# Kernel tuning notes

Hardware: AMD Instinct MI355X
Metric: run time of the kernel (lower is better)

The kernel has to match this reference:

```python
import jax, jax.numpy as jnp
import numpy as np

EMBED = 768; HEADS = 12; MLP = 3072
WL_IN = 4        # activation bits (signed)
WL_W = 4         # weight bits (bit-sliced into 1-bit RRAM cells)
ADC = 5          # ADC precision for each analog partial sum
SUBARRAY = 128   # crossbar subArray rows
ONOFF = 10.0     # conductance on/off ratio
VARI = 0.02      # conductance variability
EPS = 1e-5


def _adc_quant(y, bits):
    # Linear ADC quantization over the full observed range.
    ymax = jnp.max(jnp.abs(y))
    step = ymax / (2 ** bits - 1)
    step = jnp.where(step > 0, step, jnp.ones_like(step))
    return jnp.round(y / step) * step


def _qlinear(x, W, b, key):
    # RRAM crossbar simulated linear layer. x: [T, Fin], W: [Fout, Fin].
    upper, lower = 1.0, 1.0 / ONOFF
    T, Fin = x.shape
    Fout = W.shape[0]
    Wlev = 2 ** WL_W - 1
    Xlev = 2 ** (WL_IN - 1) - 1
    # --- weight -> unsigned integer levels -> binary cell conductances ---
    wmax = jnp.max(jnp.abs(W))
    Wdec = jnp.round((W / wmax + 1.0) * 0.5 * Wlev).astype(jnp.int32)   # [Fout,Fin] in [0,Wlev]
    kb = jnp.arange(WL_W)
    wbits = ((Wdec[:, :, None] >> kb) & 1).astype(x.dtype)              # [Fout,Fin,K]
    noise = VARI * jax.random.normal(key, wbits.shape, dtype=x.dtype)   # conductance variability
    cond = (wbits * (upper - lower) + lower) * (1.0 + noise)
    dummy = 0.5 * (upper + lower)                                       # dummy column conductance
    # --- activation -> signed integer -> magnitude bit slices ---
    xmax = jnp.max(jnp.abs(x))
    Xq = jnp.round(x / xmax * Xlev).astype(jnp.int32)
    sgn = jnp.sign(Xq).astype(x.dtype)
    zb = jnp.arange(WL_IN - 1)
    xbits = ((jnp.abs(Xq)[:, :, None] >> zb) & 1).astype(x.dtype) * sgn[:, :, None]  # [T,Fin,Z]
    # --- subArray partitioning along input dim ---
    pad = (-Fin) % SUBARRAY
    if pad:
        xbits = jnp.pad(xbits, ((0, 0), (0, pad), (0, 0)))
        cond = jnp.pad(cond, ((0, 0), (0, pad), (0, 0)))
    nc = (Fin + pad) // SUBARRAY
    xb = xbits.reshape(T, nc, SUBARRAY, WL_IN - 1)
    cb = cond.reshape(Fout, nc, SUBARRAY, WL_W)
    # analog MAC per subarray, per (input bit z, weight cell k)
    partial = jnp.einsum('tcsz,ocsk->tcozk', xb, cb)                    # [T,nc,Fout,Z,K]
    dummyP = dummy * xb.sum(axis=2)                                     # [T,nc,Z]
    partialQ = _adc_quant(partial, ADC)
    dummyQ = _adc_quant(dummyP, ADC)
    net = partialQ - dummyQ[:, :, None, :, None]                        # recenter to signed weights
    scale = (2.0 ** zb)[:, None] * (2.0 ** kb)[None, :]                 # [Z,K] shift-add
    acc = jnp.einsum('tcozk,zk->to', net, scale)
    out = acc * (xmax / Xlev) * (2.0 * wmax / ((upper - lower) * Wlev))
    return out + b


def _layernorm(x, g, b):
    mu = jnp.mean(x, axis=-1, keepdims=True)
    var = jnp.var(x, axis=-1, keepdims=True)
    return (x - mu) * jax.lax.rsqrt(var + EPS) * g + b


def _attention(x, in_w, in_b, out_w, out_b):
    L, N, E = x.shape
    D = E // HEADS
    qkv = x @ in_w.T + in_b                                             # [L,N,3E]
    q, k, v = jnp.split(qkv, 3, axis=-1)
    q = q.reshape(L, N, HEADS, D)
    k = k.reshape(L, N, HEADS, D)
    v = v.reshape(L, N, HEADS, D)
    scores = jnp.einsum('lnhd,mnhd->nhlm', q, k) / jnp.sqrt(jnp.asarray(D, x.dtype))
    attn = jax.nn.softmax(scores, axis=-1)
    ctx = jnp.einsum('nhlm,mnhd->lnhd', attn, v).reshape(L, N, E)
    return ctx @ out_w.T + out_b


def setup_inputs() -> dict:
    key = jax.random.key(0)
    ks = jax.random.split(key, 8)
    s = 0.02
    return {
        'x': jax.random.normal(ks[0], (256, 2, EMBED), jnp.float32),
        'in_proj_w': s * jax.random.normal(ks[1], (3 * EMBED, EMBED), jnp.float32),
        'in_proj_b': jnp.zeros((3 * EMBED,), jnp.float32),
        'out_proj_w': s * jax.random.normal(ks[2], (EMBED, EMBED), jnp.float32),
        'out_proj_b': jnp.zeros((EMBED,), jnp.float32),
        'ln1_g': jnp.ones((EMBED,), jnp.float32),
        'ln1_b': jnp.zeros((EMBED,), jnp.float32),
        'W1': s * jax.random.normal(ks[3], (MLP, EMBED), jnp.float32),
        'b1': jnp.zeros((MLP,), jnp.float32),
        'W2': s * jax.random.normal(ks[4], (EMBED, MLP), jnp.float32),
        'b2': jnp.zeros((EMBED,), jnp.float32),
        'ln2_g': jnp.ones((EMBED,), jnp.float32),
        'ln2_b': jnp.zeros((EMBED,), jnp.float32),
    }


def reference(x, in_proj_w, in_proj_b, out_proj_w, out_proj_b,
              ln1_g, ln1_b, W1, b1, W2, b2, ln2_g, ln2_b):
    L, N, E = x.shape
    a = _attention(x, in_proj_w, in_proj_b, out_proj_w, out_proj_b)
    h = _layernorm(x + a, ln1_g, ln1_b)
    t = h.reshape(L * N, E)
    m = _qlinear(t, W1, b1, jax.random.key(1))
    m = jax.nn.gelu(m, approximate=False)   # torch nn.GELU default = exact erf
    m = _qlinear(m, W2, b2, jax.random.key(2))
    m = m.reshape(L, N, E)
    return _layernorm(h + m, ln2_g, ln2_b)
```

## Files before the change

kernel.cpp:

```cpp
#include <hip/hip_runtime.h>
#include <math.h>
#include <stdint.h>

#define TOK   512
#define EMB   768
#define QKVD  2304
#define NHEAD 12
#define HD    64
#define MLPD  3072
#define SUBA  128

#define OFF_QKV      0ull
#define OFF_SCORES   9437184ull
#define OFF_CTX      22020096ull
#define OFF_H1PRE    25165824ull
#define OFF_H1       26738688ull
#define OFF_M1       28311552ull
#define OFF_X2       34603008ull
#define OFF_M2       40894464ull
#define OFF_DQ1      42467328ull
#define OFF_DQ2      42504192ull
#define OFF_SCAL     42651648ull
#define OFF_NOISE1   42651712ull
#define OFF_NOISE2   80400448ull
#define OFF_SUMXB1   118149184ull
#define OFF_SUMXB2   118186048ull
#define OFF_WDEC1    118333504ull
#define OFF_WDEC2    120692800ull
#define OFF_XQT1     123052096ull
#define OFF_XQT2     123445312ull
#define WS_NEEDED    125018176ull


typedef float f32x2 __attribute__((ext_vector_type(2)));

__device__ __forceinline__ f32x2 pkfma(f32x2 a, f32x2 b, f32x2 c){
#if __has_builtin(__builtin_elementwise_fma)
  return __builtin_elementwise_fma(a, b, c);
#else
  f32x2 r; r.x = fmaf(a.x, b.x, c.x); r.y = fmaf(a.y, b.y, c.y); return r;
#endif
}

__device__ __forceinline__ void blockMaxAtomic(double v, unsigned long long* slot, double* red){
  int tid = threadIdx.x;
  red[tid] = v; __syncthreads();
  for (int st = 128; st > 0; st >>= 1){
    if (tid < st){ double o = red[tid+st]; if (o > red[tid]) red[tid] = o; }
    __syncthreads();
  }
  if (tid == 0) atomicMax(slot, (unsigned long long)__double_as_longlong(red[0]));
}

__device__ __forceinline__ double readSlot(const unsigned long long* s){
  return __longlong_as_double((long long)(*s));
}

__device__ __forceinline__ float xla_exp_f32(float _x){
  float x = fminf(_x, 88.3762626647950f);
  x = fmaxf(x, -88.3762626647949f);
  float m = floorf(fmaf(x, 1.44269504088896341f, 0.5f));
  float r = fmaf(m, -0.6931471805599453f, x);
  float r2 = __fmul_rn(r, r);
  float r3 = __fmul_rn(r2, r);
  float y  = fmaf(1.9875691500e-4f, r, 1.3981999507e-3f);
  float y1 = fmaf(4.1665795894e-2f, r, 1.6666665459e-1f);
  float y2 = __fadd_rn(r, 1.0f);
  y  = fmaf(y, r, 8.3334519073e-3f);
  y1 = fmaf(y1, r, 5.0000001201e-1f);
  y  = fmaf(y, r3, y1);
  y  = fmaf(y, r2, y2);
  int mi = (int)m;
  float two_m = __uint_as_float((unsigned)((mi + 127) << 23));
  float res = __fmul_rn(y, two_m);
  return fmaxf(res, _x);
}

__device__ __forceinline__ float xla_erf_f32(float v){
  float x = fmaxf(fminf(v, 4.0f), -4.0f);
  float x2 = __fmul_rn(x, x);
  float p = fmaf(x2, -2.72614225801306e-10f, 2.77068142495902e-08f);
  p = fmaf(x2, p, -2.10102402082508e-06f);
  p = fmaf(x2, p, -5.69250639462346e-05f);
  p = fmaf(x2, p, -7.34990630326855e-04f);
  p = fmaf(x2, p, -2.95459980854025e-03f);
  p = fmaf(x2, p, -1.60960333262415e-02f);
  p = __fmul_rn(x, p);
  float q = fmaf(x2, -1.45660718464996e-05f, -2.13374055278905e-04f);
  q = fmaf(x2, q, -1.68282697438203e-03f);
  q = fmaf(x2, q, -7.37332916720468e-03f);
  q = fmaf(x2, q, -1.42647390514189e-02f);
  return __fdiv_rn(p, q);
}

__device__ __forceinline__ uint32_t rotl32(uint32_t x, int r){ return (x << r) | (x >> (32 - r)); }

__device__ __forceinline__ void threefry2x32(uint32_t k0, uint32_t k1,
                                             uint32_t x0, uint32_t x1,
                                             uint32_t& o0, uint32_t& o1){
  uint32_t ks2 = k0 ^ k1 ^ 0x1BD11BDAu;
  x0 += k0; x1 += k1;
#define TF_R(r) { x0 += x1; x1 = rotl32(x1, r); x1 ^= x0; }
  TF_R(13) TF_R(15) TF_R(26) TF_R(6)
  x0 += k1; x1 += ks2 + 1u;
  TF_R(17) TF_R(29) TF_R(16) TF_R(24)
  x0 += ks2; x1 += k0 + 2u;
  TF_R(13) TF_R(15) TF_R(26) TF_R(6)
  x0 += k0; x1 += k1 + 3u;
  TF_R(17) TF_R(29) TF_R(16) TF_R(24)
  x0 += k1; x1 += ks2 + 4u;
  TF_R(13) TF_R(15) TF_R(26) TF_R(6)
  x0 += ks2; x1 += k0 + 5u;
#undef TF_R
  o0 = x0; o1 = x1;
}

__device__ float bits_to_noise(uint32_t bits){
  uint32_t fb = (bits >> 9) | 0x3f800000u;
  float f = __uint_as_float(fb);
  f = __fadd_rn(f, -1.0f);
  const float lo = -0.99999994f;
  float u = __fadd_rn(__fmul_rn(f, 2.0f), lo);
  u = fmaxf(lo, u);
  float x  = u;
  float xx = __fmul_rn(x, x);
  float nx = -xx;
  float l1p;
  if (fabsf(nx) < 1e-4f){
    l1p = __fmul_rn(__fadd_rn(__fmul_rn(-0.5f, nx), 1.0f), nx);
  } else {
    float u1 = __fadd_rn(nx, 1.0f);
    l1p = (float)log((double)u1);
  }
  float w = -l1p;
  float p;
  if (w < 5.0f){
    w = __fadd_rn(w, -2.5f);
    p = 2.81022636e-08f;
    p = __fadd_rn(3.43273939e-07f, __fmul_rn(p, w));
    p = __fadd_rn(-3.5233877e-06f,  __fmul_rn(p, w));
    p = __fadd_rn(-4.39150654e-06f, __fmul_rn(p, w));
    p = __fadd_rn(0.00021858087f,   __fmul_rn(p, w));
    p = __fadd_rn(-0.00125372503f,  __fmul_rn(p, w));
    p = __fadd_rn(-0.00417768164f,  __fmul_rn(p, w));
    p = __fadd_rn(0.246640727f,     __fmul_rn(p, w));
    p = __fadd_rn(1.50140941f,      __fmul_rn(p, w));
  } else {
    float sw = __fsqrt_rn(w);
    w = __fadd_rn(sw, -3.0f);
    p = -0.000200214257f;
    p = __fadd_rn(0.000100950558f, __fmul_rn(p, w));
    p = __fadd_rn(0.00134934322f,  __fmul_rn(p, w));
    p = __fadd_rn(-0.00367342844f, __fmul_rn(p, w));
    p = __fadd_rn(0.00573950773f,  __fmul_rn(p, w));
    p = __fadd_rn(-0.0076224613f,  __fmul_rn(p, w));
    p = __fadd_rn(0.00943887047f,  __fmul_rn(p, w));
    p = __fadd_rn(1.00167406f,     __fmul_rn(p, w));
    p = __fadd_rn(2.83297682f,     __fmul_rn(p, w));
  }
  float ei  = __fmul_rn(p, x);
  float nrm = __fmul_rn(1.41421354f, ei);
  return __fmul_rn(0.02f, nrm);
}

__global__ void absmax_f32_k(const float* p, int n, unsigned long long* slot){
  __shared__ double red[256];
  double m = 0.0;
  for (int i = blockIdx.x*256 + threadIdx.x; i < n; i += gridDim.x*256){
    double v = fabs((double)p[i]); if (v > m) m = v;
  }
  blockMaxAtomic(m, slot, red);
}

__global__ void noise_gen_k(uint32_t k0, uint32_t k1, unsigned int n, float* noise){
  unsigned int i = blockIdx.x*256u + threadIdx.x;
  if (i >= n) return;
  uint32_t o0, o1;
  threefry2x32(k0, k1, 0u, i, o0, o1);
  noise[i] = bits_to_noise(o0 ^ o1);
}

__global__ void wdec_gen_k(const float* W, int nW, const unsigned long long* wmax_slot,
                           unsigned char* Wdec){
  int i = blockIdx.x*256 + threadIdx.x;
  if (i >= nW) return;
  float wmax = (float)readSlot(wmax_slot);
  float d = __fdiv_rn(W[i], wmax);
  d = __fadd_rn(d, 1.0f);
  d = __fmul_rn(d, 0.5f);
  d = __fmul_rn(d, 15.0f);
  Wdec[i] = (unsigned char)(int)rintf(d);
}

#define KTILE 32
__global__ __launch_bounds__(256) void gemm8_k(const float* src, const float* w, const float* bias,
                                               const float* resid, float* out, int N, int K){
  __shared__ float xt[EMB*8];
  __shared__ float wl[256*(KTILE+1)];
  const int tid = threadIdx.x;
  const int j  = blockIdx.x*256 + tid;
  const int t0 = blockIdx.y*8;
  for (int v = tid; v < K*8; v += 256){
    int e = v >> 3, tt = v & 7;
    xt[v] = src[(size_t)(t0+tt)*K + e];
  }
  f32x2 acc[4] = {{0.f,0.f},{0.f,0.f},{0.f,0.f},{0.f,0.f}};
  const int ntile = K / KTILE;
  for (int et = 0; et < ntile; ++et){
    __syncthreads();
    for (int v = tid; v < 256*KTILE; v += 256){
      int r = v >> 5, cc = v & 31;
      wl[r*(KTILE+1) + cc] = w[(size_t)(blockIdx.x*256 + r)*K + et*KTILE + cc];
    }
    __syncthreads();
    for (int ee = 0; ee < KTILE; ++ee){
      float wv = wl[tid*(KTILE+1) + ee];
      f32x2 wv2 = {wv, wv};
      const f32x2* xp = (const f32x2*)&xt[(et*KTILE + ee)*8];
#pragma unroll
      for (int q = 0; q < 4; ++q) acc[q] = pkfma(xp[q], wv2, acc[q]);
    }
  }
  float bv = bias[j];
#pragma unroll
  for (int q = 0; q < 4; ++q){
    float a0 = __fadd_rn(acc[q].x, bv);
    float a1 = __fadd_rn(acc[q].y, bv);
    size_t ta = (size_t)(t0 + q*2), tb = ta + 1;
    if (resid){
      out[ta*N + j] = __fadd_rn(resid[ta*N + j], a0);
      out[tb*N + j] = __fadd_rn(resid[tb*N + j], a1);
    } else {
      out[ta*N + j] = a0;
      out[tb*N + j] = a1;
    }
  }
}

__global__ __launch_bounds__(256) void attn_scores_k(const float* qkv, float* sc){
  __shared__ float kt[64][34];
  int nh = blockIdx.x;
  int n  = nh / NHEAD, h = nh % NHEAD;
  int m0 = blockIdx.y * 32;
  int l  = threadIdx.x;
  for (int v = threadIdx.x; v < 32*64; v += 256){
    int mm = v >> 6, d = v & 63;
    kt[d][mm] = qkv[(size_t)((m0+mm)*2 + n)*QKVD + EMB + h*HD + d];
  }
  __syncthreads();
  f32x2 acc[16];
#pragma unroll
  for (int i = 0; i < 16; ++i) acc[i] = {0.f,0.f};
  const float* qrow = qkv + (size_t)(l*2 + n)*QKVD + h*HD;
  for (int d = 0; d < HD; ++d){
    float qv = qrow[d];
    f32x2 q2 = {qv, qv};
    const f32x2* kp = (const f32x2*)&kt[d][0];
#pragma unroll
    for (int i = 0; i < 16; ++i) acc[i] = pkfma(q2, kp[i], acc[i]);
  }
  float* srow = sc + ((size_t)nh*256 + l)*256 + m0;
#pragma unroll
  for (int i = 0; i < 16; ++i){
    srow[2*i]   = __fdiv_rn(acc[i].x, 8.0f);
    srow[2*i+1] = __fdiv_rn(acc[i].y, 8.0f);
  }
}

__global__ void softmax_rows_k(float* sc){
  int row = blockIdx.x*256 + threadIdx.x;
  if (row >= 24*256) return;
  float* p = sc + (size_t)row*256;
  float mx = p[0];
  for (int m = 1; m < 256; ++m) mx = fmaxf(mx, p[m]);
  for (int m = 0; m < 256; ++m) p[m] = xla_exp_f32(__fsub_rn(p[m], mx));
  float s = 0.0f;
  for (int m = 0; m < 256; ++m) s = __fadd_rn(s, p[m]);
  for (int m = 0; m < 256; ++m) p[m] = __fdiv_rn(p[m], s);
}

__global__ void attn_ctx_k(const float* sc, const float* qkv, float* ctx){
  int idx = blockIdx.x*256 + threadIdx.x;
  int t = idx / 384, i2 = idx % 384;
  int i = i2*2;
  int l = t >> 1, n = t & 1, h = i >> 6;
  const float* arow = sc + ((size_t)(n*NHEAD + h)*256 + l)*256;
  f32x2 acc = {0.f,0.f};
  for (int m = 0; m < 256; ++m){
    float av = arow[m];
    f32x2 a2 = {av, av};
    f32x2 v2 = *(const f32x2*)&qkv[(size_t)(m*2 + n)*QKVD + 1536 + i];
    acc = pkfma(a2, v2, acc);
  }
  ctx[(size_t)t*EMB + i]     = acc.x;
  ctx[(size_t)t*EMB + i + 1] = acc.y;
}

__global__ void ln_rows_k(const float* in, const float* g, const float* b, float* out){
  int t = blockIdx.x*256 + threadIdx.x;
  if (t >= TOK) return;
  const float* p = in + (size_t)t*EMB;
  float s = 0.0f;
  for (int e = 0; e < EMB; ++e) s = __fadd_rn(s, p[e]);
  float mu = __fdiv_rn(s, 768.0f);
  float s2 = 0.0f;
  for (int e = 0; e < EMB; ++e){
    float d = __fsub_rn(p[e], mu);
    s2 = __fadd_rn(s2, __fmul_rn(d, d));
  }
  float var = __fdiv_rn(s2, 768.0f);
  float rs = __fdiv_rn(1.0f, __fsqrt_rn(__fadd_rn(var, 1e-5f)));
  for (int e = 0; e < EMB; ++e){
    float d = __fsub_rn(p[e], mu);
    out[(size_t)t*EMB + e] = __fadd_rn(__fmul_rn(__fmul_rn(d, rs), g[e]), b[e]);
  }
}

__global__ void final_ln_rows_k(const float* h1, const float* m2T, const float* g, const float* b, float* out){
  int t = blockIdx.x*256 + threadIdx.x;
  if (t >= TOK) return;
  const float* p = h1 + (size_t)t*EMB;
  float s = 0.0f;
  for (int e = 0; e < EMB; ++e) s = __fadd_rn(s, __fadd_rn(p[e], m2T[(size_t)e*TOK + t]));
  float mu = __fdiv_rn(s, 768.0f);
  float s2 = 0.0f;
  for (int e = 0; e < EMB; ++e){
    float d = __fsub_rn(__fadd_rn(p[e], m2T[(size_t)e*TOK + t]), mu);
    s2 = __fadd_rn(s2, __fmul_rn(d, d));
  }
  float var = __fdiv_rn(s2, 768.0f);
  float rs = __fdiv_rn(1.0f, __fsqrt_rn(__fadd_rn(var, 1e-5f)));
  for (int e = 0; e < EMB; ++e){
    float d = __fsub_rn(__fadd_rn(p[e], m2T[(size_t)e*TOK + t]), mu);
    out[(size_t)t*EMB + e] = __fadd_rn(__fmul_rn(__fmul_rn(d, rs), g[e]), b[e]);
  }
}

__global__ void quantx_k(const float* val, const unsigned long long* xmax_slot, int Fin,
                         signed char* XqT){
  int idx = blockIdx.x*256 + threadIdx.x;
  if (idx >= TOK*Fin) return;
  int t = idx / Fin, i = idx % Fin;
  float xmax = (float)readSlot(xmax_slot);
  float u = __fmul_rn(__fdiv_rn(val[idx], xmax), 7.0f);
  XqT[(size_t)i*TOK + t] = (signed char)(int)rintf(u);
}

__global__ void quantxT_k(const float* valT, const unsigned long long* xmax_slot, int n,
                          signed char* XqT){
  int idx = blockIdx.x*256 + threadIdx.x;
  if (idx >= n) return;
  float xmax = (float)readSlot(xmax_slot);
  float u = __fmul_rn(__fdiv_rn(valT[idx], xmax), 7.0f);
  XqT[idx] = (signed char)(int)rintf(u);
}

__global__ void sumxb_k(const signed char* XqT, int NC, int* sumxb, unsigned long long* dmax_slot){
  int idx = blockIdx.x*256 + threadIdx.x;
  if (idx >= TOK*NC) return;
  int t = idx / NC, c = idx % NC;
  int n0 = 0, n1 = 0, n2 = 0;
  for (int s = 0; s < SUBA; ++s){
    int q = XqT[(size_t)(c*SUBA + s)*TOK + t];
    int a = q < 0 ? -q : q;
    int sg = (q > 0) - (q < 0);
    n0 += (a & 1) * sg; n1 += ((a >> 1) & 1) * sg; n2 += ((a >> 2) & 1) * sg;
  }
  sumxb[idx*3 + 0] = n0; sumxb[idx*3 + 1] = n1; sumxb[idx*3 + 2] = n2;
  float d0 = fabsf(__fmul_rn(0.55f, (float)n0));
  float d1 = fabsf(__fmul_rn(0.55f, (float)n1));
  float d2 = fabsf(__fmul_rn(0.55f, (float)n2));
  float m = fmaxf(d0, fmaxf(d1, d2));
  atomicMax(dmax_slot, (unsigned long long)__double_as_longlong((double)m));
}

__global__ void dummyq_k(const int* sumxb, int NC, const unsigned long long* dmax_slot, float* dqT){
  int idx = blockIdx.x*256 + threadIdx.x;
  if (idx >= TOK*NC*3) return;
  int t = idx / (NC*3);
  int r = idx % (NC*3);
  int c = r / 3, z = r % 3;
  float dmax = (float)readSlot(dmax_slot);
  float step = __fdiv_rn(dmax, 31.0f);
  if (!(step > 0.0f)) step = 1.0f;
  float P = __fmul_rn(0.55f, (float)sumxb[idx]);
  dqT[((size_t)c*3 + z)*TOK + t] = __fmul_rn(rintf(__fdiv_rn(P, step)), step);
}

template<int OTILE>
__device__ __forceinline__ void qlin_stage(const signed char* XqT, const unsigned char* Wdec,
                                           const float* noise, int Fin, int c, int o0, int t0,
                                           signed char* xq, float (*cond)[SUBA][4]){
  const int tid = threadIdx.x;
  const uint32_t* src = (const uint32_t*)(XqT + (size_t)c*SUBA*TOK + t0);
  uint32_t* dst = (uint32_t*)xq;
  for (int j = tid; j < SUBA*64; j += 256){
    int s = j >> 6, dw = j & 63;
    dst[s*64 + dw] = src[s*128 + dw];
  }
  for (int v = tid; v < OTILE*SUBA*4; v += 256){
    int o = v >> 9;
    int r = v & 511;
    int s = r >> 2, k = r & 3;
    size_t i = (size_t)(o0+o)*Fin + c*SUBA + s;
    float bit = (float)((Wdec[i] >> k) & 1);
    float nz  = noise[i*4 + k];
    cond[o][s][k] = __fmul_rn(__fadd_rn(__fmul_rn(bit, 0.9f), 0.1f), __fadd_rn(1.0f, nz));
  }
}

template<int OTILE>
__device__ __forceinline__ void qlin_acc_c(const signed char* xq, const float (*cond)[SUBA][4],
                                           f32x2 (*acc)[6]){
  const int tid = threadIdx.x;
#pragma unroll
  for (int o = 0; o < OTILE; ++o)
#pragma unroll
    for (int r = 0; r < 6; ++r) acc[o][r] = {0.f,0.f};
  for (int s = 0; s < SUBA; ++s){
    int q = xq[s*256 + tid];
    int a = q < 0 ? -q : q;
    int i0 = a & 1, i1 = (a >> 1) & 1, i2 = (a >> 2) & 1;
    if (q < 0){ i0 = -i0; i1 = -i1; i2 = -i2; }
    float f0 = (float)i0, f1 = (float)i1, f2 = (float)i2;
    f32x2 b0 = {f0, f0}, b1 = {f1, f1}, b2 = {f2, f2};
#pragma unroll
    for (int o = 0; o < OTILE; ++o){
      const f32x2* cp = (const f32x2*)&cond[o][s][0];
      f32x2 c01 = cp[0], c23 = cp[1];
      acc[o][0] = pkfma(b0, c01, acc[o][0]);
      acc[o][1] = pkfma(b0, c23, acc[o][1]);
      acc[o][2] = pkfma(b1, c01, acc[o][2]);
      acc[o][3] = pkfma(b1, c23, acc[o][3]);
      acc[o][4] = pkfma(b2, c01, acc[o][4]);
      acc[o][5] = pkfma(b2, c23, acc[o][5]);
    }
  }
}

template<int OTILE, int CCHUNK>
__global__ __launch_bounds__(256) void qlin_pass1_t(const signed char* XqT, const unsigned char* Wdec,
                                                    const float* noise, int Fin,
                                                    unsigned long long* ymax_slot){
  __shared__ signed char xq[SUBA*256];
  __shared__ float cond[OTILE][SUBA][4];
  __shared__ double red[256];
  const int o0 = blockIdx.x*OTILE;
  const int t0 = blockIdx.y*256;
  const int c0 = blockIdx.z*CCHUNK;
  f32x2 acc[OTILE][6];
  float lmax = 0.0f;
  for (int c = c0; c < c0 + CCHUNK; ++c){
    __syncthreads();
    qlin_stage<OTILE>(XqT, Wdec, noise, Fin, c, o0, t0, xq, cond);
    __syncthreads();
    qlin_acc_c<OTILE>(xq, cond, acc);
#pragma unroll
    for (int o = 0; o < OTILE; ++o)
#pragma unroll
      for (int r = 0; r < 6; ++r){
        lmax = fmaxf(lmax, fabsf(acc[o][r].x));
        lmax = fmaxf(lmax, fabsf(acc[o][r].y));
      }
  }
  blockMaxAtomic((double)lmax, ymax_slot, red);
}

template<int OTILE>
__global__ __launch_bounds__(256) void qlin_pass2_t(const signed char* XqT, const unsigned char* Wdec,
                                                    const float* noise, const float* dqT, const float* bias,
                                                    int Fin, int NC,
                                                    const unsigned long long* ymax_slot,
                                                    const unsigned long long* xmax_slot,
                                                    const unsigned long long* wmax_slot,
                                                    float* outT){
  __shared__ signed char xq[SUBA*256];
  __shared__ float cond[OTILE][SUBA][4];
  const int o0 = blockIdx.x*OTILE;
  const int t0 = blockIdx.y*256;
  const int t  = t0 + threadIdx.x;
  float ymax = (float)readSlot(ymax_slot);
  float step = __fdiv_rn(ymax, 31.0f);
  if (!(step > 0.0f)) step = 1.0f;
  f32x2 acc[OTILE][6];
  float netsum[OTILE][12];
#pragma unroll
  for (int o = 0; o < OTILE; ++o)
#pragma unroll
    for (int r = 0; r < 12; ++r) netsum[o][r] = 0.0f;
  for (int c = 0; c < NC; ++c){
    __syncthreads();
    qlin_stage<OTILE>(XqT, Wdec, noise, Fin, c, o0, t0, xq, cond);
    __syncthreads();
    qlin_acc_c<OTILE>(xq, cond, acc);
    float dqv[3];
#pragma unroll
    for (int z = 0; z < 3; ++z) dqv[z] = dqT[((size_t)c*3 + z)*TOK + t];
#pragma unroll
    for (int o = 0; o < OTILE; ++o)
#pragma unroll
      for (int z = 0; z < 3; ++z)
#pragma unroll
        for (int k = 0; k < 4; ++k){
          f32x2 av2 = acc[o][z*2 + (k >> 1)];
          float av = (k & 1) ? av2.y : av2.x;
          float pq  = __fmul_rn(rintf(__fdiv_rn(av, step)), step);
          float net = __fsub_rn(pq, dqv[z]);
          netsum[o][z*4+k] = __fadd_rn(netsum[o][z*4+k], net);
        }
  }
  float xmax = (float)readSlot(xmax_slot);
  float wmax = (float)readSlot(wmax_slot);
  float A = __fdiv_rn(xmax, 7.0f);
  float B = __fdiv_rn(__fmul_rn(2.0f, wmax), 13.5f);
#pragma unroll
  for (int o = 0; o < OTILE; ++o){
    float tot = 0.0f;
#pragma unroll
    for (int z = 0; z < 3; ++z)
#pragma unroll
      for (int k = 0; k < 4; ++k)
        tot = __fadd_rn(tot, __fmul_rn(netsum[o][z*4+k], (float)(1 << (z + k))));
    float outv = __fadd_rn(__fmul_rn(__fmul_rn(tot, A), B), bias[o0+o]);
    outT[(size_t)(o0+o)*TOK + t] = outv;
  }
}

__global__ void gelu_absmax_k(const float* m1, int n, float* x2, unsigned long long* xmax_slot){
  __shared__ double red[256];
  double m = 0.0;
  for (int i = blockIdx.x*256 + threadIdx.x; i < n; i += gridDim.x*256){
    float v = m1[i];
    float t1 = __fdiv_rn(v, 1.4142135623730951f);
    float e = xla_erf_f32(t1);
    float s = __fadd_rn(e, 1.0f);
    float g = __fdiv_rn(__fmul_rn(v, s), 2.0f);
    x2[i] = g;
    double a = fabs((double)g); if (a > m) m = a;
  }
  blockMaxAtomic(m, xmax_slot, red);
}

extern "C" void kernel_launch(void* const* d_in, const int* in_sizes, int n_in,
                              void* d_out, int out_size, void* d_ws, size_t ws_size,
                              hipStream_t stream){
  if (ws_size < WS_NEEDED) return;
  const float* x      = (const float*)d_in[0];
  const float* in_w   = (const float*)d_in[1];
  const float* in_b   = (const float*)d_in[2];
  const float* out_w  = (const float*)d_in[3];
  const float* out_b  = (const float*)d_in[4];
  const float* ln1_g  = (const float*)d_in[5];
  const float* ln1_b  = (const float*)d_in[6];
  const float* W1     = (const float*)d_in[7];
  const float* b1     = (const float*)d_in[8];
  const float* W2     = (const float*)d_in[9];
  const float* b2     = (const float*)d_in[10];
  const float* ln2_g  = (const float*)d_in[11];
  const float* ln2_b  = (const float*)d_in[12];

  char* ws = (char*)d_ws;
  float* qkv    = (float*)(ws + OFF_QKV);
  float* scores = (float*)(ws + OFF_SCORES);
  float* ctx    = (float*)(ws + OFF_CTX);
  float* h1pre  = (float*)(ws + OFF_H1PRE);
  float* h1     = (float*)(ws + OFF_H1);
  float* m1     = (float*)(ws + OFF_M1);
  float* x2     = (float*)(ws + OFF_X2);
  float* m2     = (float*)(ws + OFF_M2);
  float* dq1    = (float*)(ws + OFF_DQ1);
  float* dq2    = (float*)(ws + OFF_DQ2);
  unsigned long long* scal = (unsigned long long*)(ws + OFF_SCAL);
  float* noise1  = (float*)(ws + OFF_NOISE1);
  float* noise2  = (float*)(ws + OFF_NOISE2);
  int*   sumxb1  = (int*)(ws + OFF_SUMXB1);
  int*   sumxb2  = (int*)(ws + OFF_SUMXB2);
  unsigned char* wdec1 = (unsigned char*)(ws + OFF_WDEC1);
  unsigned char* wdec2 = (unsigned char*)(ws + OFF_WDEC2);
  signed char* xqt1 = (signed char*)(ws + OFF_XQT1);
  signed char* xqt2 = (signed char*)(ws + OFF_XQT2);

  hipMemsetAsync(scal, 0, 64, stream);

  absmax_f32_k<<<1024,256,0,stream>>>(W1, MLPD*EMB, scal+0);
  absmax_f32_k<<<1024,256,0,stream>>>(W2, EMB*MLPD, scal+1);

  noise_gen_k<<<36864,256,0,stream>>>(0u, 1u, 9437184u, noise1);
  noise_gen_k<<<36864,256,0,stream>>>(0u, 2u, 9437184u, noise2);
  wdec_gen_k<<<9216,256,0,stream>>>(W1, MLPD*EMB, scal+0, wdec1);
  wdec_gen_k<<<9216,256,0,stream>>>(W2, EMB*MLPD, scal+1, wdec2);

  gemm8_k<<<dim3(9,64),256,0,stream>>>(x, in_w, in_b, nullptr, qkv, QKVD, EMB);
  attn_scores_k<<<dim3(24,8),256,0,stream>>>(qkv, scores);
  softmax_rows_k<<<24,256,0,stream>>>(scores);
  attn_ctx_k<<<768,256,0,stream>>>(scores, qkv, ctx);
  gemm8_k<<<dim3(3,64),256,0,stream>>>(ctx, out_w, out_b, x, h1pre, EMB, EMB);
  ln_rows_k<<<2,256,0,stream>>>(h1pre, ln1_g, ln1_b, h1);

  absmax_f32_k<<<1024,256,0,stream>>>(h1, TOK*EMB, scal+2);
  quantx_k<<<(TOK*EMB+255)/256,256,0,stream>>>(h1, scal+2, EMB, xqt1);
  sumxb_k<<<(TOK*6+255)/256,256,0,stream>>>(xqt1, 6, sumxb1, scal+4);
  dummyq_k<<<(TOK*6*3+255)/256,256,0,stream>>>(sumxb1, 6, scal+4, dq1);
  qlin_pass1_t<8,3><<<dim3(MLPD/8,2,2),256,0,stream>>>(xqt1, wdec1, noise1, EMB, scal+3);
  qlin_pass2_t<4><<<dim3(MLPD/4,2),256,0,stream>>>(xqt1, wdec1, noise1, dq1, b1,
                                                   EMB, 6, scal+3, scal+2, scal+0, m1);

  gelu_absmax_k<<<6144,256,0,stream>>>(m1, TOK*MLPD, x2, scal+5);
  quantxT_k<<<(TOK*MLPD+255)/256,256,0,stream>>>(x2, scal+5, TOK*MLPD, xqt2);
  sumxb_k<<<(TOK*24+255)/256,256,0,stream>>>(xqt2, 24, sumxb2, scal+7);
  dummyq_k<<<(TOK*24*3+255)/256,256,0,stream>>>(sumxb2, 24, scal+7, dq2);
  qlin_pass1_t<4,6><<<dim3(EMB/4,2,4),256,0,stream>>>(xqt2, wdec2, noise2, MLPD, scal+6);
  qlin_pass2_t<4><<<dim3(EMB/4,2),256,0,stream>>>(xqt2, wdec2, noise2, dq2, b2,
                                                  MLPD, 24, scal+6, scal+5, scal+1, m2);

  final_ln_rows_k<<<2,256,0,stream>>>(h1, m2, ln2_g, ln2_b, (float*)d_out);
}
```

Before: 3.149 ms.

## Precompute crossbar conductances once and register-prefetch them in unified qlin kernel

Fuses noise generation with weight bit-slicing into a single cond_gen kernel that writes final conductance values, so the qlin kernels load ready float4 conductances instead of recomputing them from Wdec and noise in every pass. The activation quant layout becomes token-major per subarray, so each thread reads its own 128 activations directly from global memory instead of staging them through shared memory. Pass1 and pass2 are merged into one templated kernel that prefetches the next chunk's conductances into registers while computing the current one. The pk_fma is forced through inline asm. This trades a larger workspace and more register pressure for fewer shared-memory stages and less redundant per-pass work.

```diff
diff --git a/kernel.cpp b/kernel.cpp
--- a/kernel.cpp
+++ b/kernel.cpp
@@ -10,36 +10,34 @@
 #define MLPD  3072
 #define SUBA  128
 
-#define OFF_QKV      0ull
-#define OFF_SCORES   9437184ull
-#define OFF_CTX      22020096ull
-#define OFF_H1PRE    25165824ull
-#define OFF_H1       26738688ull
-#define OFF_M1       28311552ull
-#define OFF_X2       34603008ull
-#define OFF_M2       40894464ull
-#define OFF_DQ1      42467328ull
-#define OFF_DQ2      42504192ull
-#define OFF_SCAL     42651648ull
-#define OFF_NOISE1   42651712ull
-#define OFF_NOISE2   80400448ull
-#define OFF_SUMXB1   118149184ull
-#define OFF_SUMXB2   118186048ull
-#define OFF_WDEC1    118333504ull
-#define OFF_WDEC2    120692800ull
-#define OFF_XQT1     123052096ull
-#define OFF_XQT2     123445312ull
-#define WS_NEEDED    125018176ull
+#define OFF_SCAL     0ull
+#define OFF_QKV      256ull
+#define OFF_SCORES   (OFF_QKV    + 4718592ull)
+#define OFF_CTX      (OFF_SCORES + 6291456ull)
+#define OFF_H1PRE    (OFF_CTX    + 1572864ull)
+#define OFF_H1       (OFF_H1PRE  + 1572864ull)
+#define OFF_M1       (OFF_H1     + 1572864ull)
+#define OFF_X2       (OFF_M1     + 6291456ull)
+#define OFF_M2       (OFF_X2     + 6291456ull)
+#define OFF_DQ1      (OFF_M2     + 1572864ull)
+#define OFF_DQ2      (OFF_DQ1    + 36864ull)
+#define OFF_SUMXB1   (OFF_DQ2    + 147456ull)
+#define OFF_SUMXB2   (OFF_SUMXB1 + 36864ull)
+#define OFF_WDEC1    (OFF_SUMXB2 + 147456ull)
+#define OFF_WDEC2    (OFF_WDEC1  + 2359296ull)
+#define OFF_XQT1     (OFF_WDEC2  + 2359296ull)
+#define OFF_XQT2     (OFF_XQT1   + 393216ull)
+#define OFF_COND1    (OFF_XQT2   + 1572864ull)
+#define OFF_COND2    (OFF_COND1  + 37748736ull)
+#define WS_NEEDED    (OFF_COND2  + 37748736ull)
 
 
 typedef float f32x2 __attribute__((ext_vector_type(2)));
 
 __device__ __forceinline__ f32x2 pkfma(f32x2 a, f32x2 b, f32x2 c){
-#if __has_builtin(__builtin_elementwise_fma)
-  return __builtin_elementwise_fma(a, b, c);
-#else
-  f32x2 r; r.x = fmaf(a.x, b.x, c.x); r.y = fmaf(a.y, b.y, c.y); return r;
-#endif
+  f32x2 d;
+  asm("v_pk_fma_f32 %0, %1, %2, %3" : "=v"(d) : "v"(a), "v"(b), "v"(c));
+  return d;
 }
 
 __device__ __forceinline__ void blockMaxAtomic(double v, unsigned long long* slot, double* red){
@@ -172,14 +170,6 @@
   blockMaxAtomic(m, slot, red);
 }
 
-__global__ void noise_gen_k(uint32_t k0, uint32_t k1, unsigned int n, float* noise){
-  unsigned int i = blockIdx.x*256u + threadIdx.x;
-  if (i >= n) return;
-  uint32_t o0, o1;
-  threefry2x32(k0, k1, 0u, i, o0, o1);
-  noise[i] = bits_to_noise(o0 ^ o1);
-}
-
 __global__ void wdec_gen_k(const float* W, int nW, const unsigned long long* wmax_slot,
                            unsigned char* Wdec){
   int i = blockIdx.x*256 + threadIdx.x;
@@ -190,6 +180,17 @@
   d = __fmul_rn(d, 0.5f);
   d = __fmul_rn(d, 15.0f);
   Wdec[i] = (unsigned char)(int)rintf(d);
+}
+
+__global__ void cond_gen_k(uint32_t k0, uint32_t k1, const unsigned char* Wdec,
+                           unsigned int n4, float* cond){
+  unsigned int j = blockIdx.x*256u + threadIdx.x;
+  if (j >= n4) return;
+  uint32_t o0, o1;
+  threefry2x32(k0, k1, 0u, j, o0, o1);
+  float nz = bits_to_noise(o0 ^ o1);
+  float bit = (float)((Wdec[j >> 2] >> (j & 3)) & 1);
+  cond[j] = __fmul_rn(__fadd_rn(__fmul_rn(bit, 0.9f), 0.1f), __fadd_rn(1.0f, nz));
 }
 
 #define KTILE 32
@@ -336,32 +337,34 @@
   }
 }
 
-__global__ void quantx_k(const float* val, const unsigned long long* xmax_slot, int Fin,
-                         signed char* XqT){
+__global__ void quantx_k(const float* val , const unsigned long long* xmax_slot,
+                         int Fin, signed char* XqT2){
   int idx = blockIdx.x*256 + threadIdx.x;
   if (idx >= TOK*Fin) return;
-  int t = idx / Fin, i = idx % Fin;
+  int t = idx / Fin, e = idx % Fin;
   float xmax = (float)readSlot(xmax_slot);
   float u = __fmul_rn(__fdiv_rn(val[idx], xmax), 7.0f);
-  XqT[(size_t)i*TOK + t] = (signed char)(int)rintf(u);
-}
-
-__global__ void quantxT_k(const float* valT, const unsigned long long* xmax_slot, int n,
-                          signed char* XqT){
+  XqT2[((size_t)(e >> 7)*TOK + t)*SUBA + (e & 127)] = (signed char)(int)rintf(u);
+}
+
+__global__ void quantxT_k(const float* valT , const unsigned long long* xmax_slot,
+                          int Fin, signed char* XqT2){
   int idx = blockIdx.x*256 + threadIdx.x;
-  if (idx >= n) return;
+  if (idx >= TOK*Fin) return;
+  int i = idx / TOK, t = idx % TOK;
   float xmax = (float)readSlot(xmax_slot);
   float u = __fmul_rn(__fdiv_rn(valT[idx], xmax), 7.0f);
-  XqT[idx] = (signed char)(int)rintf(u);
-}
-
-__global__ void sumxb_k(const signed char* XqT, int NC, int* sumxb, unsigned long long* dmax_slot){
+  XqT2[((size_t)(i >> 7)*TOK + t)*SUBA + (i & 127)] = (signed char)(int)rintf(u);
+}
+
+__global__ void sumxb_k(const signed char* XqT2, int NC, int* sumxb, unsigned long long* dmax_slot){
   int idx = blockIdx.x*256 + threadIdx.x;
   if (idx >= TOK*NC) return;
   int t = idx / NC, c = idx % NC;
+  const signed char* row = XqT2 + ((size_t)c*TOK + t)*SUBA;
   int n0 = 0, n1 = 0, n2 = 0;
   for (int s = 0; s < SUBA; ++s){
-    int q = XqT[(size_t)(c*SUBA + s)*TOK + t];
+    int q = row[s];
     int a = q < 0 ? -q : q;
     int sg = (q > 0) - (q < 0);
     n0 += (a & 1) * sg; n1 += ((a >> 1) & 1) * sg; n2 += ((a >> 2) & 1) * sg;
@@ -387,142 +390,161 @@
   dqT[((size_t)c*3 + z)*TOK + t] = __fmul_rn(rintf(__fdiv_rn(P, step)), step);
 }
 
-template<int OTILE>
-__device__ __forceinline__ void qlin_stage(const signed char* XqT, const unsigned char* Wdec,
-                                           const float* noise, int Fin, int c, int o0, int t0,
-                                           signed char* xq, float (*cond)[SUBA][4]){
+template<int OTILE, bool P2, int CCHUNK>
+__global__ __launch_bounds__(256) void qlin_k(const signed char* XqT2, const float* cond_g,
+                                              const float* dqT, const float* bias,
+                                              int Fin, int NC,
+                                              unsigned long long* ymax_slot,
+                                              const unsigned long long* xmax_slot,
+                                              const unsigned long long* wmax_slot,
+                                              float* outT){
+  __shared__ float condL[OTILE*SUBA*4];
+  __shared__ double red[256];
   const int tid = threadIdx.x;
-  const uint32_t* src = (const uint32_t*)(XqT + (size_t)c*SUBA*TOK + t0);
-  uint32_t* dst = (uint32_t*)xq;
-  for (int j = tid; j < SUBA*64; j += 256){
-    int s = j >> 6, dw = j & 63;
-    dst[s*64 + dw] = src[s*128 + dw];
-  }
-  for (int v = tid; v < OTILE*SUBA*4; v += 256){
-    int o = v >> 9;
-    int r = v & 511;
-    int s = r >> 2, k = r & 3;
-    size_t i = (size_t)(o0+o)*Fin + c*SUBA + s;
-    float bit = (float)((Wdec[i] >> k) & 1);
-    float nz  = noise[i*4 + k];
-    cond[o][s][k] = __fmul_rn(__fadd_rn(__fmul_rn(bit, 0.9f), 0.1f), __fadd_rn(1.0f, nz));
-  }
-}
-
-template<int OTILE>
-__device__ __forceinline__ void qlin_acc_c(const signed char* xq, const float (*cond)[SUBA][4],
-                                           f32x2 (*acc)[6]){
-  const int tid = threadIdx.x;
-#pragma unroll
-  for (int o = 0; o < OTILE; ++o)
-#pragma unroll
-    for (int r = 0; r < 6; ++r) acc[o][r] = {0.f,0.f};
-  for (int s = 0; s < SUBA; ++s){
-    int q = xq[s*256 + tid];
-    int a = q < 0 ? -q : q;
-    int i0 = a & 1, i1 = (a >> 1) & 1, i2 = (a >> 2) & 1;
-    if (q < 0){ i0 = -i0; i1 = -i1; i2 = -i2; }
-    float f0 = (float)i0, f1 = (float)i1, f2 = (float)i2;
-    f32x2 b0 = {f0, f0}, b1 = {f1, f1}, b2 = {f2, f2};
-#pragma unroll
-    for (int o = 0; o < OTILE; ++o){
-      const f32x2* cp = (const f32x2*)&cond[o][s][0];
-      f32x2 c01 = cp[0], c23 = cp[1];
-      acc[o][0] = pkfma(b0, c01, acc[o][0]);
-      acc[o][1] = pkfma(b0, c23, acc[o][1]);
-      acc[o][2] = pkfma(b1, c01, acc[o][2]);
-      acc[o][3] = pkfma(b1, c23, acc[o][3]);
-      acc[o][4] = pkfma(b2, c01, acc[o][4]);
-      acc[o][5] = pkfma(b2, c23, acc[o][5]);
-    }
-  }
-}
-
-template<int OTILE, int CCHUNK>
-__global__ __launch_bounds__(256) void qlin_pass1_t(const signed char* XqT, const unsigned char* Wdec,
-                                                    const float* noise, int Fin,
-                                                    unsigned long long* ymax_slot){
-  __shared__ signed char xq[SUBA*256];
-  __shared__ float cond[OTILE][SUBA][4];
-  __shared__ double red[256];
   const int o0 = blockIdx.x*OTILE;
   const int t0 = blockIdx.y*256;
-  const int c0 = blockIdx.z*CCHUNK;
+  const int t  = t0 + tid;
+  const int c0 = P2 ? 0 : blockIdx.z*CCHUNK;
+  const int cEnd = P2 ? NC : (c0 + CCHUNK);
+
+  float step = 1.0f, lmax = 0.0f;
+  if (P2){
+    float ymax = (float)readSlot(ymax_slot);
+    step = __fdiv_rn(ymax, 31.0f);
+    if (!(step > 0.0f)) step = 1.0f;
+  }
+
   f32x2 acc[OTILE][6];
-  float lmax = 0.0f;
-  for (int c = c0; c < c0 + CCHUNK; ++c){
+  f32x2 netsum[OTILE][6];
+  if (P2){
+#pragma unroll
+    for (int o = 0; o < OTILE; ++o)
+#pragma unroll
+      for (int r = 0; r < 6; ++r) netsum[o][r] = (f32x2){0.f, 0.f};
+  }
+
+#pragma unroll
+  for (int u = 0; u < OTILE/2; ++u){
+    int v = tid + u*256, o = v >> 7, r = v & 127;
+    ((float4*)condL)[v] = ((const float4*)cond_g)[(size_t)(o0+o)*Fin + (size_t)c0*SUBA + r];
+  }
+  __syncthreads();
+
+  for (int c = c0; c < cEnd; ++c){
+    const uint32_t* xrow = (const uint32_t*)(XqT2 + ((size_t)c*TOK + t)*SUBA);
+    uint32_t xg[8];
+#pragma unroll
+    for (int u = 0; u < 8; ++u) xg[u] = xrow[u];
+
+    float4 pf[OTILE/2];
+    const bool havePF = (c + 1 < cEnd);
+    if (havePF){
+#pragma unroll
+      for (int u = 0; u < OTILE/2; ++u){
+        int v = tid + u*256, o = v >> 7, r = v & 127;
+        pf[u] = ((const float4*)cond_g)[(size_t)(o0+o)*Fin + (size_t)(c+1)*SUBA + r];
+      }
+    }
+
+#pragma unroll
+    for (int o = 0; o < OTILE; ++o)
+#pragma unroll
+      for (int r = 0; r < 6; ++r) acc[o][r] = (f32x2){0.f, 0.f};
+
+    for (int g = 0; g < 4; ++g){
+      uint32_t xn[8];
+      if (g < 3){
+#pragma unroll
+        for (int u = 0; u < 8; ++u) xn[u] = xrow[(g+1)*8 + u];
+      }
+      const float* condG = condL + g*32*4;
+#pragma unroll
+      for (int u = 0; u < 8; ++u){
+        uint32_t w = xg[u];
+#pragma unroll
+        for (int bb = 0; bb < 4; ++bb){
+          int sl = u*4 + bb;
+          int q = (int)(signed char)(w >> (8*bb));
+          int a = q < 0 ? -q : q;
+          int i0 = a & 1, i1 = (a >> 1) & 1, i2 = (a >> 2) & 1;
+          if (q < 0){ i0 = -i0; i1 = -i1; i2 = -i2; }
+          float f0 = (float)i0, f1 = (float)i1, f2 = (float)i2;
+          f32x2 b0 = {f0, f0}, b1 = {f1, f1}, b2 = {f2, f2};
+#pragma unroll
+          for (int o = 0; o < OTILE; ++o){
+            const f32x2* cp = (const f32x2*)&condG[(o*SUBA + sl)*4];
+            f32x2 c01 = cp[0], c23 = cp[1];
+            acc[o][0] = pkfma(b0, c01, acc[o][0]);
+            acc[o][1] = pkfma(b0, c23, acc[o][1]);
+            acc[o][2] = pkfma(b1, c01, acc[o][2]);
+            acc[o][3] = pkfma(b1, c23, acc[o][3]);
+            acc[o][4] = pkfma(b2, c01, acc[o][4]);
+            acc[o][5] = pkfma(b2, c23, acc[o][5]);
+          }
+        }
+      }
+      if (g < 3){
+#pragma unroll
+        for (int u = 0; u < 8; ++u) xg[u] = xn[u];
+      }
+    }
+
+    if (P2){
+      float dqv[3];
+#pragma unroll
+      for (int z = 0; z < 3; ++z) dqv[z] = dqT[((size_t)c*3 + z)*TOK + t];
+#pragma unroll
+      for (int o = 0; o < OTILE; ++o)
+#pragma unroll
+        for (int z = 0; z < 3; ++z)
+#pragma unroll
+          for (int kp = 0; kp < 2; ++kp){
+            f32x2 av = acc[o][z*2 + kp];
+            float pq0 = __fmul_rn(rintf(__fdiv_rn(av.x, step)), step);
+            float pq1 = __fmul_rn(rintf(__fdiv_rn(av.y, step)), step);
+            netsum[o][z*2+kp].x = __fadd_rn(netsum[o][z*2+kp].x, __fsub_rn(pq0, dqv[z]));
+            netsum[o][z*2+kp].y = __fadd_rn(netsum[o][z*2+kp].y, __fsub_rn(pq1, dqv[z]));
+          }
+    } else {
+#pragma unroll
+      for (int o = 0; o < OTILE; ++o)
+#pragma unroll
+        for (int r = 0; r < 6; ++r){
+          lmax = fmaxf(lmax, fabsf(acc[o][r].x));
+          lmax = fmaxf(lmax, fabsf(acc[o][r].y));
+        }
+    }
+
     __syncthreads();
-    qlin_stage<OTILE>(XqT, Wdec, noise, Fin, c, o0, t0, xq, cond);
-    __syncthreads();
-    qlin_acc_c<OTILE>(xq, cond, acc);
-#pragma unroll
-    for (int o = 0; o < OTILE; ++o)
-#pragma unroll
-      for (int r = 0; r < 6; ++r){
-        lmax = fmaxf(lmax, fabsf(acc[o][r].x));
-        lmax = fmaxf(lmax, fabsf(acc[o][r].y));
-      }
-  }
-  blockMaxAtomic((double)lmax, ymax_slot, red);
-}
-
-template<int OTILE>
-__global__ __launch_bounds__(256) void qlin_pass2_t(const signed char* XqT, const unsigned char* Wdec,
-                                                    const float* noise, const float* dqT, const float* bias,
-                                                    int Fin, int NC,
-                                                    const unsigned long long* ymax_slot,
-                                                    const unsigned long long* xmax_slot,
-                                                    const unsigned long long* wmax_slot,
-                                                    float* outT){
-  __shared__ signed char xq[SUBA*256];
-  __shared__ float cond[OTILE][SUBA][4];
-  const int o0 = blockIdx.x*OTILE;
-  const int t0 = blockIdx.y*256;
-  const int t  = t0 + threadIdx.x;
-  float ymax = (float)readSlot(ymax_slot);
-  float step = __fdiv_rn(ymax, 31.0f);
-  if (!(step > 0.0f)) step = 1.0f;
-  f32x2 acc[OTILE][6];
-  float netsum[OTILE][12];
-#pragma unroll
-  for (int o = 0; o < OTILE; ++o)
-#pragma unroll
-    for (int r = 0; r < 12; ++r) netsum[o][r] = 0.0f;
-  for (int c = 0; c < NC; ++c){
-    __syncthreads();
-    qlin_stage<OTILE>(XqT, Wdec, noise, Fin, c, o0, t0, xq, cond);
-    __syncthreads();
-    qlin_acc_c<OTILE>(xq, cond, acc);
-    float dqv[3];
-#pragma unroll
-    for (int z = 0; z < 3; ++z) dqv[z] = dqT[((size_t)c*3 + z)*TOK + t];
-#pragma unroll
-    for (int o = 0; o < OTILE; ++o)
+    if (havePF){
+#pragma unroll
+      for (int u = 0; u < OTILE/2; ++u)
+        ((float4*)condL)[tid + u*256] = pf[u];
+      __syncthreads();
+    }
+  }
+
+  if (P2){
+    float xmax = (float)readSlot(xmax_slot);
+    float wmax = (float)readSlot(wmax_slot);
+    float A = __fdiv_rn(xmax, 7.0f);
+    float B = __fdiv_rn(__fmul_rn(2.0f, wmax), 13.5f);
+#pragma unroll
+    for (int o = 0; o < OTILE; ++o){
+      float tot = 0.0f;
 #pragma unroll
       for (int z = 0; z < 3; ++z)
 #pragma unroll
         for (int k = 0; k < 4; ++k){
-          f32x2 av2 = acc[o][z*2 + (k >> 1)];
-          float av = (k & 1) ? av2.y : av2.x;
-          float pq  = __fmul_rn(rintf(__fdiv_rn(av, step)), step);
-          float net = __fsub_rn(pq, dqv[z]);
-          netsum[o][z*4+k] = __fadd_rn(netsum[o][z*4+k], net);
+          f32x2 ns = netsum[o][z*2 + (k >> 1)];
+          float nv = (k & 1) ? ns.y : ns.x;
+          tot = __fadd_rn(tot, __fmul_rn(nv, (float)(1 << (z + k))));
         }
-  }
-  float xmax = (float)readSlot(xmax_slot);
-  float wmax = (float)readSlot(wmax_slot);
-  float A = __fdiv_rn(xmax, 7.0f);
-  float B = __fdiv_rn(__fmul_rn(2.0f, wmax), 13.5f);
-#pragma unroll
-  for (int o = 0; o < OTILE; ++o){
-    float tot = 0.0f;
-#pragma unroll
-    for (int z = 0; z < 3; ++z)
-#pragma unroll
-      for (int k = 0; k < 4; ++k)
-        tot = __fadd_rn(tot, __fmul_rn(netsum[o][z*4+k], (float)(1 << (z + k))));
-    float outv = __fadd_rn(__fmul_rn(__fmul_rn(tot, A), B), bias[o0+o]);
-    outT[(size_t)(o0+o)*TOK + t] = outv;
+      float outv = __fadd_rn(__fmul_rn(__fmul_rn(tot, A), B), bias[o0+o]);
+      outT[(size_t)(o0+o)*TOK + t] = outv;
+    }
+  } else {
+    blockMaxAtomic((double)lmax, ymax_slot, red);
   }
 }
 
@@ -560,6 +582,7 @@
   const float* ln2_b  = (const float*)d_in[12];
 
   char* ws = (char*)d_ws;
+  unsigned long long* scal = (unsigned long long*)(ws + OFF_SCAL);
   float* qkv    = (float*)(ws + OFF_QKV);
   float* scores = (float*)(ws + OFF_SCORES);
   float* ctx    = (float*)(ws + OFF_CTX);
@@ -570,25 +593,23 @@
   float* m2     = (float*)(ws + OFF_M2);
   float* dq1    = (float*)(ws + OFF_DQ1);
   float* dq2    = (float*)(ws + OFF_DQ2);
-  unsigned long long* scal = (unsigned long long*)(ws + OFF_SCAL);
-  float* noise1  = (float*)(ws + OFF_NOISE1);
-  float* noise2  = (float*)(ws + OFF_NOISE2);
-  int*   sumxb1  = (int*)(ws + OFF_SUMXB1);
-  int*   sumxb2  = (int*)(ws + OFF_SUMXB2);
+  int*   sumxb1 = (int*)(ws + OFF_SUMXB1);
+  int*   sumxb2 = (int*)(ws + OFF_SUMXB2);
   unsigned char* wdec1 = (unsigned char*)(ws + OFF_WDEC1);
   unsigned char* wdec2 = (unsigned char*)(ws + OFF_WDEC2);
   signed char* xqt1 = (signed char*)(ws + OFF_XQT1);
   signed char* xqt2 = (signed char*)(ws + OFF_XQT2);
+  float* cond1 = (float*)(ws + OFF_COND1);
+  float* cond2 = (float*)(ws + OFF_COND2);
 
   hipMemsetAsync(scal, 0, 64, stream);
 
   absmax_f32_k<<<1024,256,0,stream>>>(W1, MLPD*EMB, scal+0);
   absmax_f32_k<<<1024,256,0,stream>>>(W2, EMB*MLPD, scal+1);
-
-  noise_gen_k<<<36864,256,0,stream>>>(0u, 1u, 9437184u, noise1);
-  noise_gen_k<<<36864,256,0,stream>>>(0u, 2u, 9437184u, noise2);
   wdec_gen_k<<<9216,256,0,stream>>>(W1, MLPD*EMB, scal+0, wdec1);
   wdec_gen_k<<<9216,256,0,stream>>>(W2, EMB*MLPD, scal+1, wdec2);
+  cond_gen_k<<<36864,256,0,stream>>>(0u, 1u, wdec1, 9437184u, cond1);
+  cond_gen_k<<<36864,256,0,stream>>>(0u, 2u, wdec2, 9437184u, cond2);
 
   gemm8_k<<<dim3(9,64),256,0,stream>>>(x, in_w, in_b, nullptr, qkv, QKVD, EMB);
   attn_scores_k<<<dim3(24,8),256,0,stream>>>(qkv, scores);
@@ -601,17 +622,19 @@
   quantx_k<<<(TOK*EMB+255)/256,256,0,stream>>>(h1, scal+2, EMB, xqt1);
   sumxb_k<<<(TOK*6+255)/256,256,0,stream>>>(xqt1, 6, sumxb1, scal+4);
   dummyq_k<<<(TOK*6*3+255)/256,256,0,stream>>>(sumxb1, 6, scal+4, dq1);
-  qlin_pass1_t<8,3><<<dim3(MLPD/8,2,2),256,0,stream>>>(xqt1, wdec1, noise1, EMB, scal+3);
-  qlin_pass2_t<4><<<dim3(MLPD/4,2),256,0,stream>>>(xqt1, wdec1, noise1, dq1, b1,
-                                                   EMB, 6, scal+3, scal+2, scal+0, m1);
+  qlin_k<4,false,3><<<dim3(MLPD/4,2,2),256,0,stream>>>(xqt1, cond1, nullptr, nullptr,
+                                                       EMB, 6, scal+3, scal+2, scal+0, nullptr);
+  qlin_k<4,true,1><<<dim3(MLPD/4,2),256,0,stream>>>(xqt1, cond1, dq1, b1,
+                                                    EMB, 6, scal+3, scal+2, scal+0, m1);
 
   gelu_absmax_k<<<6144,256,0,stream>>>(m1, TOK*MLPD, x2, scal+5);
-  quantxT_k<<<(TOK*MLPD+255)/256,256,0,stream>>>(x2, scal+5, TOK*MLPD, xqt2);
+  quantxT_k<<<(TOK*MLPD+255)/256,256,0,stream>>>(x2, scal+5, MLPD, xqt2);
   sumxb_k<<<(TOK*24+255)/256,256,0,stream>>>(xqt2, 24, sumxb2, scal+7);
   dummyq_k<<<(TOK*24*3+255)/256,256,0,stream>>>(sumxb2, 24, scal+7, dq2);
-  qlin_pass1_t<4,6><<<dim3(EMB/4,2,4),256,0,stream>>>(xqt2, wdec2, noise2, MLPD, scal+6);
-  qlin_pass2_t<4><<<dim3(EMB/4,2),256,0,stream>>>(xqt2, wdec2, noise2, dq2, b2,
-                                                  MLPD, 24, scal+6, scal+5, scal+1, m2);
+  qlin_k<4,false,6><<<dim3(EMB/4,2,4),256,0,stream>>>(xqt2, cond2, nullptr, nullptr,
+                                                      MLPD, 24, scal+6, scal+5, scal+1, nullptr);
+  qlin_k<4,true,1><<<dim3(EMB/4,2),256,0,stream>>>(xqt2, cond2, dq2, b2,
+                                                   MLPD, 24, scal+6, scal+5, scal+1, m2);
 
   final_ln_rows_k<<<2,256,0,stream>>>(h1, m2, ln2_g, ln2_b, (float*)d_out);
 }
```

After: 3.201 ms. No clear change (+1.6%).
